# Performance work log

Hardware: AMD Instinct MI355X
Metric: run time of the kernel (lower is better)

Reference implementation:

```python
import jax, jax.numpy as jnp
import numpy as np
from functools import partial

N = 10000      # nodes
E = 100000     # edges
WIDTH = 64     # node hidden width
KER_W = 1024   # kernel MLP hidden width
KER_IN = 6     # edge feature dim
DEPTH = 6


def setup_inputs() -> dict:
    key = jax.random.key(0)
    ks = jax.random.split(key, 16)

    def glorot(k, shape):
        fan_in = shape[0]
        return jax.random.normal(k, shape, dtype=jnp.float32) / np.sqrt(fan_in)

    inp = {
        "x": jax.random.normal(ks[0], (N, 1), dtype=jnp.float32),
        "edge_index": jax.random.randint(ks[1], (2, E), 0, N, dtype=jnp.int32),
        "edge_attr": jax.random.uniform(ks[2], (E, KER_IN), dtype=jnp.float32),
        # fc1: in_width=1 -> width
        "fc1_w": glorot(ks[3], (1, WIDTH)),
        "fc1_b": jnp.zeros((WIDTH,), jnp.float32),
        # kernel DenseNet: ker_in -> ker_width -> ker_width -> width**2 (ReLU between)
        "k1_w": glorot(ks[4], (KER_IN, KER_W)),
        "k1_b": jnp.zeros((KER_W,), jnp.float32),
        "k2_w": glorot(ks[5], (KER_W, KER_W)),
        "k2_b": jnp.zeros((KER_W,), jnp.float32),
        "k3_w": glorot(ks[6], (KER_W, WIDTH * WIDTH)),
        "k3_b": jnp.zeros((WIDTH * WIDTH,), jnp.float32),
        # NNConv_old root weight + bias
        "root_w": glorot(ks[7], (WIDTH, WIDTH)),
        "conv_b": jnp.zeros((WIDTH,), jnp.float32),
        # fc2: width -> 1
        "fc2_w": glorot(ks[8], (WIDTH, 1)),
        "fc2_b": jnp.zeros((1,), jnp.float32),
    }
    return inp


def reference(x, edge_index, edge_attr, fc1_w, fc1_b, k1_w, k1_b, k2_w, k2_b,
              k3_w, k3_b, root_w, conv_b, fc2_w, fc2_b):
    src = edge_index[0]  # x_j (source, gathered)
    dst = edge_index[1]  # aggregation target

    # Per-edge kernel MLP -> [E, width, width]. edge_attr is constant across
    # depth iterations, so compute the edge weights once (same math).
    h = jax.nn.relu(edge_attr @ k1_w + k1_b)
    h = jax.nn.relu(h @ k2_w + k2_b)
    ew = (h @ k3_w + k3_b).reshape(E, WIDTH, WIDTH)

    # mean aggregation denominators (scatter_mean semantics: deg clamped to 1)
    deg = jax.ops.segment_sum(jnp.ones((E,), jnp.float32), dst, num_segments=N)
    deg = jnp.maximum(deg, 1.0)[:, None]  # [N,1]

    z = x @ fc1_w + fc1_b  # [N, width]
    for _ in range(DEPTH):
        msg = jnp.einsum('ei,eio->eo', z[src], ew)            # gather + per-edge matmul
        agg = jax.ops.segment_sum(msg, dst, num_segments=N)   # scatter-add
        agg = agg / deg                                       # mean
        z = jax.nn.relu(agg + z @ root_w + conv_b)
    return z @ fc2_w + fc2_b  # [N, 1]
```

## Files before the change

### kernel.cpp

```cpp
#include <hip/hip_runtime.h>
#include <hip/hip_bf16.h>

#define N_NODES 10000
#define N_EDGES 100000
#define DEPTH   6
#define E_CHUNK 12500

typedef __attribute__((ext_vector_type(8))) short short8;
typedef __attribute__((ext_vector_type(4))) float f32x4;
typedef unsigned short u16;

__device__ __forceinline__ float bf2f(u16 u) {
    union { float f; unsigned int i; } v; v.i = ((unsigned int)u) << 16; return v.f;
}
__device__ __forceinline__ u16 f2bf(float f) {
    union { float f; unsigned int i; } v; v.f = f;
    unsigned int x = v.i;
    unsigned int r = (x + 0x7fffu + ((x >> 16) & 1u)) >> 16;
    return (u16)r;
}

__device__ __forceinline__ void gload_lds16(const void* g, void* s) {
    __builtin_amdgcn_global_load_lds((const __attribute__((address_space(1))) void*)g,
                                     (__attribute__((address_space(3))) void*)s, 16, 0, 0);
}

__global__ void k2_transpose_kernel(const float* __restrict__ k2w, u16* __restrict__ k2T) {
    int idx = blockIdx.x * 256 + threadIdx.x;
    int n = idx >> 10, k = idx & 1023;
    k2T[idx] = f2bf(k2w[k * 1024 + n]);
}
__global__ void k3_permT_kernel(const float* __restrict__ k3w, u16* __restrict__ k3pT) {
    int idx = blockIdx.x * 256 + threadIdx.x;
    int n = idx >> 10, c = idx & 1023;
    k3pT[idx] = f2bf(k3w[(size_t)c * 4096 + (n & 63) * 64 + (n >> 6)]);
}
__global__ void b3_permute_kernel(const float* __restrict__ b3, float* __restrict__ b3p) {
    int n = blockIdx.x * 256 + threadIdx.x;
    if (n >= 4096) return;
    b3p[n] = b3[(n & 63) * 64 + (n >> 6)];
}

__global__ void deg_kernel(const int* __restrict__ ei, float* __restrict__ deg) {
    int e = blockIdx.x * 256 + threadIdx.x;
    if (e < N_EDGES) atomicAdd(&deg[ei[N_EDGES + e]], 1.0f);
}

__global__ void gemm1_kernel(const float* __restrict__ ea, const float* __restrict__ k1w,
                             const float* __restrict__ k1b, u16* __restrict__ h1, int e0) {
    int idx = blockIdx.x * 256 + threadIdx.x;
    int c = idx & 1023;
    int e = (idx >> 10) + e0;
    float acc = k1b[c];
#pragma unroll
    for (int i = 0; i < 6; i++) acc += ea[e * 6 + i] * k1w[i * 1024 + c];
    h1[idx] = f2bf(fmaxf(acc, 0.0f));
}

template <int NOUT, bool RELU, bool FUSE_MSG>
__global__ __launch_bounds__(256) void gemm128_kernel(
    const u16* __restrict__ A, const u16* __restrict__ BT,
    const float* __restrict__ bias, u16* __restrict__ C, int M,
    const int* __restrict__ ei, const float* __restrict__ z,
    float* __restrict__ agg) {
    constexpr int K = 1024;
    constexpr int KTILES = 32;
    __shared__ __align__(16) u16 ldsA[3][128 * 32];
    __shared__ __align__(16) u16 ldsB[3][128 * 32];

    const int t = threadIdx.x;
    const int lane = t & 63, w = t >> 6;
    const int wm = w >> 1, wn = w & 1;
    const int fm = lane & 15, q = lane >> 4;
    const int m0 = blockIdx.y * 128;
    const int n0 = blockIdx.x * 128;

    f32x4 acc[4][4];
#pragma unroll
    for (int a = 0; a < 4; a++)
#pragma unroll
        for (int b = 0; b < 4; b++) acc[a][b] = (f32x4){0.f, 0.f, 0.f, 0.f};

    const u16* gA[2]; const u16* gB[2];
    int dL[2];
#pragma unroll
    for (int l = 0; l < 2; l++) {
        int L = l * 256 + t;
        int r = L >> 2;
        int kq = (L & 3) ^ ((r >> 1) & 3);
        int ra = m0 + r; if (ra >= M) ra = M - 1;
        gA[l] = A + (size_t)ra * K + kq * 8;
        gB[l] = BT + (size_t)(n0 + r) * K + kq * 8;
        dL[l] = L * 8;
    }
    const int xq = q ^ ((fm >> 1) & 3);
    const int aB = (wm * 64 + fm) * 32 + xq * 8;
    const int bB = (wn * 64 + fm) * 32 + xq * 8;

#pragma unroll
    for (int tt = 0; tt < 2; tt++) {
#pragma unroll
        for (int l = 0; l < 2; l++) { gload_lds16(gA[l], &ldsA[tt][dL[l]]); gA[l] += 32; }
#pragma unroll
        for (int l = 0; l < 2; l++) { gload_lds16(gB[l], &ldsB[tt][dL[l]]); gB[l] += 32; }
    }
    asm volatile("s_waitcnt vmcnt(4)" ::: "memory");
    __builtin_amdgcn_s_barrier();
    asm volatile("" ::: "memory");

    int cur = 0;
    for (int kt = 0; kt < KTILES; ++kt) {
        const u16* la = ldsA[cur];
        const u16* lb = ldsB[cur];

        short8 af[4], bf[4];
#pragma unroll
        for (int mi = 0; mi < 4; mi++)
            af[mi] = *reinterpret_cast<const short8*>(&la[aB + mi * 512]);
#pragma unroll
        for (int ni = 0; ni < 4; ni++)
            bf[ni] = *reinterpret_cast<const short8*>(&lb[bB + ni * 512]);

        if (kt + 2 < KTILES) {
            int nb = cur + 2; if (nb >= 3) nb -= 3;
#pragma unroll
            for (int l = 0; l < 2; l++) { gload_lds16(gA[l], &ldsA[nb][dL[l]]); gA[l] += 32; }
#pragma unroll
            for (int l = 0; l < 2; l++) { gload_lds16(gB[l], &ldsB[nb][dL[l]]); gB[l] += 32; }
        }

        __builtin_amdgcn_s_setprio(1);
#pragma unroll
        for (int mi = 0; mi < 4; mi++)
#pragma unroll
            for (int ni = 0; ni < 4; ni++)
                acc[mi][ni] = __builtin_amdgcn_mfma_f32_16x16x32_bf16(af[mi], bf[ni], acc[mi][ni], 0, 0, 0);
        __builtin_amdgcn_s_setprio(0);

        if (kt + 2 < KTILES) {
            asm volatile("s_waitcnt vmcnt(4)" ::: "memory");
        } else if (kt + 1 < KTILES) {
            asm volatile("s_waitcnt vmcnt(0)" ::: "memory");
        }
        if (kt + 1 < KTILES) {
            __builtin_amdgcn_s_barrier();
            asm volatile("" ::: "memory");
        }
        cur = cur + 1; if (cur == 3) cur = 0;
    }

    if (!FUSE_MSG) {
#pragma unroll
        for (int mi = 0; mi < 4; mi++) {
#pragma unroll
            for (int ni = 0; ni < 4; ni++) {
                int col = n0 + wn * 64 + ni * 16 + fm;
                float bsv = bias[col];
#pragma unroll
                for (int r = 0; r < 4; r++) {
                    int row = m0 + wm * 64 + mi * 16 + q * 4 + r;
                    if (row < M) {
                        float v = acc[mi][ni][r] + bsv;
                        if (RELU) v = fmaxf(v, 0.0f);
                        C[(size_t)row * NOUT + col] = f2bf(v);
                    }
                }
            }
        }
    } else {
        const int o = (n0 >> 6) + wn;
        float bsv[4];
        int iidx[4];
#pragma unroll
        for (int ni = 0; ni < 4; ni++) {
            bsv[ni] = bias[n0 + wn * 64 + ni * 16 + fm];
            iidx[ni] = ni * 16 + fm;
        }
#pragma unroll
        for (int mi = 0; mi < 4; mi++) {
#pragma unroll
            for (int r = 0; r < 4; r++) {
                int e = m0 + wm * 64 + mi * 16 + q * 4 + r;
                float partial = 0.f;
                int dst = 0;
                if (e < M) {
                    int src = ei[e];
                    dst = ei[N_EDGES + e];
                    const float* zs = z + (size_t)src * 64;
#pragma unroll
                    for (int ni = 0; ni < 4; ni++)
                        partial += (acc[mi][ni][r] + bsv[ni]) * zs[iidx[ni]];
                }
                partial += __shfl_xor(partial, 1);
                partial += __shfl_xor(partial, 2);
                partial += __shfl_xor(partial, 4);
                partial += __shfl_xor(partial, 8);
                if (fm == 0 && e < M) atomicAdd(&agg[(size_t)dst * 64 + o], partial);
            }
        }
    }
}

__global__ void z0_kernel(const float* __restrict__ x, const float* __restrict__ w,
                          const float* __restrict__ b, float* __restrict__ z) {
    int idx = blockIdx.x * 256 + threadIdx.x;
    int n = idx >> 6, o = idx & 63;
    z[idx] = x[n] * w[o] + b[o];
}

__global__ __launch_bounds__(256) void update_kernel(const float* __restrict__ zin,
                                                     const float* __restrict__ agg,
                                                     const float* __restrict__ deg,
                                                     const float* __restrict__ rootw,
                                                     const float* __restrict__ convb,
                                                     float* __restrict__ zout) {
    int n = blockIdx.x * 4 + (threadIdx.x >> 6);
    int o = threadIdx.x & 63;
    float r = convb[o];
    const float* zr = zin + (size_t)n * 64;
#pragma unroll 8
    for (int i = 0; i < 64; i++) r += zr[i] * rootw[i * 64 + o];
    float d = deg[n];
    d = d < 1.0f ? 1.0f : d;
    float v = agg[(size_t)n * 64 + o] / d + r;
    zout[(size_t)n * 64 + o] = fmaxf(v, 0.0f);
}

__global__ void final_kernel(const float* __restrict__ z, const float* __restrict__ w,
                             const float* __restrict__ b, float* __restrict__ out) {
    int n = blockIdx.x * 256 + threadIdx.x;
    if (n >= N_NODES) return;
    float acc = b[0];
#pragma unroll 8
    for (int o = 0; o < 64; o++) acc += z[(size_t)n * 64 + o] * w[o];
    out[n] = acc;
}

__global__ void dbg_kernel(float* __restrict__ out, float val, int n) {
    int i = blockIdx.x * 256 + threadIdx.x;
    if (i < n) out[i] = val;
}

extern "C" void kernel_launch(void* const* d_in, const int* in_sizes, int n_in,
                              void* d_out, int out_size, void* d_ws, size_t ws_size,
                              hipStream_t stream) {
    const float* x     = (const float*)d_in[0];
    const int*   ei    = (const int*)  d_in[1];
    const float* ea    = (const float*)d_in[2];
    const float* fc1w  = (const float*)d_in[3];
    const float* fc1b  = (const float*)d_in[4];
    const float* k1w   = (const float*)d_in[5];
    const float* k1b   = (const float*)d_in[6];
    const float* k2w   = (const float*)d_in[7];
    const float* k2b   = (const float*)d_in[8];
    const float* k3w   = (const float*)d_in[9];
    const float* k3b   = (const float*)d_in[10];
    const float* rootw = (const float*)d_in[11];
    const float* convb = (const float*)d_in[12];
    const float* fc2w  = (const float*)d_in[13];
    const float* fc2b  = (const float*)d_in[14];
    float* out = (float*)d_out;

    const size_t NEED = 249000000;
    if (ws_size < NEED) {
        dbg_kernel<<<(N_NODES + 255) / 256, 256, 0, stream>>>(out, (float)(ws_size >> 20), N_NODES);
        return;
    }

    char* p = (char*)d_ws;
    auto alloc = [&](size_t bytes) {
        char* r = p;
        p += (bytes + 255) & ~(size_t)255;
        return r;
    };
    u16*   h2   = (u16*)  alloc((size_t)N_EDGES * 1024 * 2);
    u16*   h1ch = (u16*)  alloc((size_t)E_CHUNK * 1024 * 2);
    u16*   k2T  = (u16*)  alloc((size_t)1024 * 1024 * 2);
    u16*   k3pT = (u16*)  alloc((size_t)4096 * 1024 * 2);
    float* b3p  = (float*)alloc(4096 * 4);
    float* zA   = (float*)alloc((size_t)N_NODES * 64 * 4);
    float* zB   = (float*)alloc((size_t)N_NODES * 64 * 4);
    float* agg  = (float*)alloc((size_t)N_NODES * 64 * 4);
    float* deg  = (float*)alloc((size_t)N_NODES * 4);

    hipMemsetAsync(deg, 0, (size_t)N_NODES * 4, stream);

    k2_transpose_kernel<<<(1024 * 1024) / 256, 256, 0, stream>>>(k2w, k2T);
    k3_permT_kernel<<<(4096 * 1024) / 256, 256, 0, stream>>>(k3w, k3pT);
    b3_permute_kernel<<<16, 256, 0, stream>>>(k3b, b3p);
    deg_kernel<<<(N_EDGES + 255) / 256, 256, 0, stream>>>(ei, deg);

    for (int e0 = 0; e0 < N_EDGES; e0 += E_CHUNK) {
        gemm1_kernel<<<(E_CHUNK * 1024) / 256, 256, 0, stream>>>(ea, k1w, k1b, h1ch, e0);
        dim3 g2(1024 / 128, (E_CHUNK + 127) / 128);
        gemm128_kernel<1024, true, false><<<g2, 256, 0, stream>>>(
            h1ch, k2T, k2b, h2 + (size_t)e0 * 1024, E_CHUNK, nullptr, nullptr, nullptr);
    }

    z0_kernel<<<(N_NODES * 64) / 256, 256, 0, stream>>>(x, fc1w, fc1b, zA);

    float* zin = zA;
    float* zout = zB;
    for (int d = 0; d < DEPTH; d++) {
        hipMemsetAsync(agg, 0, (size_t)N_NODES * 64 * 4, stream);
        dim3 g3(4096 / 128, (N_EDGES + 127) / 128);
        gemm128_kernel<4096, false, true><<<g3, 256, 0, stream>>>(
            h2, k3pT, b3p, nullptr, N_EDGES, ei, zin, agg);
        update_kernel<<<N_NODES / 4, 256, 0, stream>>>(zin, agg, deg, rootw, convb, zout);
        float* tmp = zin; zin = zout; zout = tmp;
    }

    final_kernel<<<(N_NODES + 255) / 256, 256, 0, stream>>>(zin, fc2w, fc2b, out);
}
```

Baseline: 7.496 ms.

## Use 256x256 tiled 8-wave fused GEMM for per-depth edge message kernel

Replaces the 128x128 fused k3 GEMM plus message-scatter kernel with a dedicated 256x256 tile kernel using 512 threads, 64-wide K slices and a double-buffered, interleaved stage/read/MFMA schedule with XOR-swizzled LDS. Larger tiles raise arithmetic intensity and cut the number of times A and B are re-read from global memory across the dominant per-depth GEMM. The cost is heavier register and LDS use per block and many barriers, which may limit occupancy. The generic GEMM loses its fused-message template branch.

```diff
diff --git a/kernel.cpp b/kernel.cpp
--- a/kernel.cpp
+++ b/kernel.cpp
@@ -57,12 +57,10 @@
     h1[idx] = f2bf(fmaxf(acc, 0.0f));
 }
 
-template <int NOUT, bool RELU, bool FUSE_MSG>
+template <int NOUT, bool RELU>
 __global__ __launch_bounds__(256) void gemm128_kernel(
     const u16* __restrict__ A, const u16* __restrict__ BT,
-    const float* __restrict__ bias, u16* __restrict__ C, int M,
-    const int* __restrict__ ei, const float* __restrict__ z,
-    float* __restrict__ agg) {
+    const float* __restrict__ bias, u16* __restrict__ C, int M) {
     constexpr int K = 1024;
     constexpr int KTILES = 32;
     __shared__ __align__(16) u16 ldsA[3][128 * 32];
@@ -149,56 +147,193 @@
         cur = cur + 1; if (cur == 3) cur = 0;
     }
 
-    if (!FUSE_MSG) {
-#pragma unroll
-        for (int mi = 0; mi < 4; mi++) {
-#pragma unroll
-            for (int ni = 0; ni < 4; ni++) {
-                int col = n0 + wn * 64 + ni * 16 + fm;
-                float bsv = bias[col];
-#pragma unroll
-                for (int r = 0; r < 4; r++) {
-                    int row = m0 + wm * 64 + mi * 16 + q * 4 + r;
-                    if (row < M) {
-                        float v = acc[mi][ni][r] + bsv;
-                        if (RELU) v = fmaxf(v, 0.0f);
-                        C[(size_t)row * NOUT + col] = f2bf(v);
-                    }
+#pragma unroll
+    for (int mi = 0; mi < 4; mi++) {
+#pragma unroll
+        for (int ni = 0; ni < 4; ni++) {
+            int col = n0 + wn * 64 + ni * 16 + fm;
+            float bsv = bias[col];
+#pragma unroll
+            for (int r = 0; r < 4; r++) {
+                int row = m0 + wm * 64 + mi * 16 + q * 4 + r;
+                if (row < M) {
+                    float v = acc[mi][ni][r] + bsv;
+                    if (RELU) v = fmaxf(v, 0.0f);
+                    C[(size_t)row * NOUT + col] = f2bf(v);
                 }
             }
         }
-    } else {
-        const int o = (n0 >> 6) + wn;
-        float bsv[4];
-        int iidx[4];
-#pragma unroll
-        for (int ni = 0; ni < 4; ni++) {
-            bsv[ni] = bias[n0 + wn * 64 + ni * 16 + fm];
-            iidx[ni] = ni * 16 + fm;
-        }
-#pragma unroll
-        for (int mi = 0; mi < 4; mi++) {
-#pragma unroll
-            for (int r = 0; r < 4; r++) {
-                int e = m0 + wm * 64 + mi * 16 + q * 4 + r;
-                float partial = 0.f;
-                int dst = 0;
-                if (e < M) {
-                    int src = ei[e];
-                    dst = ei[N_EDGES + e];
-                    const float* zs = z + (size_t)src * 64;
-#pragma unroll
-                    for (int ni = 0; ni < 4; ni++)
-                        partial += (acc[mi][ni][r] + bsv[ni]) * zs[iidx[ni]];
-                }
-                partial += __shfl_xor(partial, 1);
-                partial += __shfl_xor(partial, 2);
-                partial += __shfl_xor(partial, 4);
-                partial += __shfl_xor(partial, 8);
-                if (fm == 0 && e < M) atomicAdd(&agg[(size_t)dst * 64 + o], partial);
+    }
+}
+
+__global__ __launch_bounds__(512, 2) void fused256_kernel(
+    const u16* __restrict__ A, const u16* __restrict__ BT,
+    const float* __restrict__ bias, const int* __restrict__ ei,
+    const float* __restrict__ z, float* __restrict__ agg) {
+    __shared__ __align__(16) u16 ldsA[2 * 2 * 128 * 64];
+    __shared__ __align__(16) u16 ldsB[2 * 2 * 128 * 64];
+
+    const int t = threadIdx.x;
+    const int lane = t & 63, w = t >> 6;
+    const int wm = w >> 2, wn = w & 3;
+    const int fm = lane & 15, q = lane >> 4;
+    const int m0 = blockIdx.y * 256;
+    const int n0 = blockIdx.x * 256;
+    const int M = N_EDGES;
+
+    const u16* pA[2][2]; const u16* pB[2][2];
+    int dOff[2];
+#pragma unroll
+    for (int l = 0; l < 2; l++) {
+        int L = l * 512 + t;
+        int r = L >> 3, sp = L & 7;
+        int kofs = (sp ^ (r & 7)) * 8;
+        dOff[l] = L * 8;
+#pragma unroll
+        for (int h = 0; h < 2; h++) {
+            int ra = m0 + h * 128 + r; if (ra >= M) ra = M - 1;
+            pA[h][l] = A + (size_t)ra * 1024 + kofs;
+            pB[h][l] = BT + (size_t)(n0 + h * 128 + r) * 1024 + kofs;
+        }
+    }
+
+#define LDSA(cp, h) (ldsA + ((((cp) * 2 + (h))) << 13))
+#define LDSB(cp, h) (ldsB + ((((cp) * 2 + (h))) << 13))
+#define STAGE_A(cp, h, kofs) do { \
+        gload_lds16(pA[h][0] + (kofs), LDSA(cp, h) + dOff[0]); \
+        gload_lds16(pA[h][1] + (kofs), LDSA(cp, h) + dOff[1]); } while (0)
+#define STAGE_B(cp, h, kofs) do { \
+        gload_lds16(pB[h][0] + (kofs), LDSB(cp, h) + dOff[0]); \
+        gload_lds16(pB[h][1] + (kofs), LDSB(cp, h) + dOff[1]); } while (0)
+#define BAR() do { __builtin_amdgcn_s_barrier(); asm volatile("" ::: "memory"); } while (0)
+
+    int sslot[2];
+    sslot[0] = ((q) ^ (fm & 7)) * 8;
+    sslot[1] = ((4 + q) ^ (fm & 7)) * 8;
+    const int bh = wn >> 1;
+    const int bRow = (wn & 1) * 64 + fm;
+
+    f32x4 acc[8][4];
+#pragma unroll
+    for (int a = 0; a < 8; a++)
+#pragma unroll
+        for (int b = 0; b < 4; b++) acc[a][b] = (f32x4){0.f, 0.f, 0.f, 0.f};
+
+    short8 af[4][2], bf0[2][2], bf1[2][2];
+
+#define READ_A(cp, miB) do { \
+        _Pragma("unroll") for (int m2 = 0; m2 < 4; m2++) \
+        _Pragma("unroll") for (int ks = 0; ks < 2; ks++) \
+            af[m2][ks] = *reinterpret_cast<const short8*>( \
+                LDSA(cp, wm) + (((miB) + m2) * 16 + fm) * 64 + sslot[ks]); } while (0)
+#define READ_B(cp, reg, niB) do { \
+        _Pragma("unroll") for (int n2 = 0; n2 < 2; n2++) \
+        _Pragma("unroll") for (int ks = 0; ks < 2; ks++) \
+            reg[n2][ks] = *reinterpret_cast<const short8*>( \
+                LDSB(cp, bh) + (bRow + ((niB) + n2) * 16) * 64 + sslot[ks]); } while (0)
+#define MFMA_Q(miB, reg, niB) do { \
+        __builtin_amdgcn_s_setprio(1); \
+        _Pragma("unroll") for (int m2 = 0; m2 < 4; m2++) \
+        _Pragma("unroll") for (int n2 = 0; n2 < 2; n2++) { \
+            acc[(miB) + m2][(niB) + n2] = __builtin_amdgcn_mfma_f32_16x16x32_bf16( \
+                af[m2][0], reg[n2][0], acc[(miB) + m2][(niB) + n2], 0, 0, 0); \
+            acc[(miB) + m2][(niB) + n2] = __builtin_amdgcn_mfma_f32_16x16x32_bf16( \
+                af[m2][1], reg[n2][1], acc[(miB) + m2][(niB) + n2], 0, 0, 0); } \
+        __builtin_amdgcn_s_setprio(0); } while (0)
+
+    STAGE_A(0, 0, 0); STAGE_A(0, 1, 0); STAGE_B(0, 0, 0); STAGE_B(0, 1, 0);
+    STAGE_B(1, 0, 64); STAGE_B(1, 1, 64);
+    asm volatile("s_waitcnt vmcnt(4)" ::: "memory");
+    BAR();
+
+    for (int it = 0; it < 8; ++it) {
+        const int kB = it * 128 + 64;
+        const int kC = it * 128 + 128;
+        const int kD = it * 128 + 192;
+        const bool g = (it < 7);
+        READ_A(0, 0); READ_B(0, bf0, 0);
+        STAGE_A(1, 0, kB);
+        BAR();
+        MFMA_Q(0, bf0, 0);
+        BAR();
+        READ_B(0, bf1, 2);
+        STAGE_A(1, 1, kB);
+        BAR();
+        MFMA_Q(0, bf1, 2);
+        BAR();
+        READ_A(0, 4);
+        if (g) STAGE_B(0, 0, kC);
+        BAR();
+        MFMA_Q(4, bf1, 2);
+        BAR();
+        if (g) STAGE_B(0, 1, kC);
+        BAR();
+        MFMA_Q(4, bf0, 0);
+        if (g) { asm volatile("s_waitcnt vmcnt(4)" ::: "memory"); }
+        else   { asm volatile("s_waitcnt vmcnt(0)" ::: "memory"); }
+        BAR();
+        READ_A(1, 0); READ_B(1, bf0, 0);
+        if (g) STAGE_A(0, 0, kC);
+        BAR();
+        MFMA_Q(0, bf0, 0);
+        BAR();
+        READ_B(1, bf1, 2);
+        if (g) STAGE_A(0, 1, kC);
+        BAR();
+        MFMA_Q(0, bf1, 2);
+        BAR();
+        READ_A(1, 4);
+        if (g) STAGE_B(1, 0, kD);
+        BAR();
+        MFMA_Q(4, bf1, 2);
+        BAR();
+        if (g) STAGE_B(1, 1, kD);
+        BAR();
+        MFMA_Q(4, bf0, 0);
+        if (g) {
+            asm volatile("s_waitcnt vmcnt(4)" ::: "memory");
+            BAR();
+        }
+    }
+
+    const int o = (n0 >> 6) + wn;
+    float bsv[4];
+    int iidx[4];
+#pragma unroll
+    for (int ni = 0; ni < 4; ni++) {
+        bsv[ni] = bias[n0 + wn * 64 + ni * 16 + fm];
+        iidx[ni] = ni * 16 + fm;
+    }
+#pragma unroll
+    for (int mi = 0; mi < 8; mi++) {
+#pragma unroll
+        for (int r = 0; r < 4; r++) {
+            int e = m0 + wm * 128 + mi * 16 + q * 4 + r;
+            float partial = 0.f;
+            int dst = 0;
+            if (e < M) {
+                int src = ei[e];
+                dst = ei[N_EDGES + e];
+                const float* zs = z + (size_t)src * 64;
+#pragma unroll
+                for (int ni = 0; ni < 4; ni++)
+                    partial += (acc[mi][ni][r] + bsv[ni]) * zs[iidx[ni]];
             }
-        }
-    }
+            partial += __shfl_xor(partial, 1);
+            partial += __shfl_xor(partial, 2);
+            partial += __shfl_xor(partial, 4);
+            partial += __shfl_xor(partial, 8);
+            if (fm == 0 && e < M) atomicAdd(&agg[(size_t)dst * 64 + o], partial);
+        }
+    }
+#undef LDSA
+#undef LDSB
+#undef STAGE_A
+#undef STAGE_B
+#undef BAR
+#undef READ_A
+#undef READ_B
+#undef MFMA_Q
 }
 
 __global__ void z0_kernel(const float* __restrict__ x, const float* __restrict__ w,
@@ -293,8 +428,8 @@
     for (int e0 = 0; e0 < N_EDGES; e0 += E_CHUNK) {
         gemm1_kernel<<<(E_CHUNK * 1024) / 256, 256, 0, stream>>>(ea, k1w, k1b, h1ch, e0);
         dim3 g2(1024 / 128, (E_CHUNK + 127) / 128);
-        gemm128_kernel<1024, true, false><<<g2, 256, 0, stream>>>(
-            h1ch, k2T, k2b, h2 + (size_t)e0 * 1024, E_CHUNK, nullptr, nullptr, nullptr);
+        gemm128_kernel<1024, true><<<g2, 256, 0, stream>>>(
+            h1ch, k2T, k2b, h2 + (size_t)e0 * 1024, E_CHUNK);
     }
 
     z0_kernel<<<(N_NODES * 64) / 256, 256, 0, stream>>>(x, fc1w, fc1b, zA);
@@ -303,9 +438,8 @@
     float* zout = zB;
     for (int d = 0; d < DEPTH; d++) {
         hipMemsetAsync(agg, 0, (size_t)N_NODES * 64 * 4, stream);
-        dim3 g3(4096 / 128, (N_EDGES + 127) / 128);
-        gemm128_kernel<4096, false, true><<<g3, 256, 0, stream>>>(
-            h2, k3pT, b3p, nullptr, N_EDGES, ei, zin, agg);
+        dim3 g3(4096 / 256, (N_EDGES + 255) / 256);
+        fused256_kernel<<<g3, 512, 0, stream>>>(h2, k3pT, b3p, ei, zin, agg);
         update_kernel<<<N_NODES / 4, 256, 0, stream>>>(zin, agg, deg, rootw, convb, zout);
         float* tmp = zin; zin = zout; zout = tmp;
     }
```

Result: slower. 8.784 ms (+17.2%).

## Reassociate per-edge message via node-level z·W3 product with source-sorted edges

Applied to the files above, without the earlier changes.

Instead of materializing the per-edge 64x64 weights each depth step through a 100000x4096x1024 GEMM, the message is reassociated. Each step first computes Y = z_src·W3 per source node, a small MFMA over node blocks that uses a bf16 hi/lo split of z to keep precision. Each edge's message is then the h2 row dotted with Y, plus a precomputed bias term. Edges are sorted by source through a histogram, scan and scatter so that each block handles the edges of 16 source nodes and reuses Y from LDS. This sharply cuts the FLOPs per depth step, but it adds sort preprocessing, streaming of h2 and W3T on every step, and a large per-thread slot register array that can hurt occupancy.

```diff
diff --git a/kernel.cpp b/kernel.cpp
--- a/kernel.cpp
+++ b/kernel.cpp
@@ -5,6 +5,10 @@
 #define N_EDGES 100000
 #define DEPTH   6
 #define E_CHUNK 12500
+#define NPB     16
+#define SLOTS   48
+#define CCH     16
+#define NCH     64
 
 typedef __attribute__((ext_vector_type(8))) short short8;
 typedef __attribute__((ext_vector_type(4))) float f32x4;
@@ -30,39 +34,77 @@
     int n = idx >> 10, k = idx & 1023;
     k2T[idx] = f2bf(k2w[k * 1024 + n]);
 }
-__global__ void k3_permT_kernel(const float* __restrict__ k3w, u16* __restrict__ k3pT) {
+__global__ void w3t_kernel(const float* __restrict__ k3w, u16* __restrict__ W3T) {
     int idx = blockIdx.x * 256 + threadIdx.x;
-    int n = idx >> 10, c = idx & 1023;
-    k3pT[idx] = f2bf(k3w[(size_t)c * 4096 + (n & 63) * 64 + (n >> 6)]);
-}
-__global__ void b3_permute_kernel(const float* __restrict__ b3, float* __restrict__ b3p) {
-    int n = blockIdx.x * 256 + threadIdx.x;
-    if (n >= 4096) return;
-    b3p[n] = b3[(n & 63) * 64 + (n >> 6)];
+    int col = idx >> 6, i = idx & 63;
+    int c = col >> 6, o = col & 63;
+    W3T[idx] = f2bf(k3w[(size_t)c * 4096 + i * 64 + o]);
 }
 
 __global__ void deg_kernel(const int* __restrict__ ei, float* __restrict__ deg) {
     int e = blockIdx.x * 256 + threadIdx.x;
     if (e < N_EDGES) atomicAdd(&deg[ei[N_EDGES + e]], 1.0f);
 }
+__global__ void srchist_kernel(const int* __restrict__ ei, int* __restrict__ cnt) {
+    int e = blockIdx.x * 256 + threadIdx.x;
+    if (e < N_EDGES) atomicAdd(&cnt[ei[e]], 1);
+}
+__global__ void scan_kernel(const int* __restrict__ cnt, int* __restrict__ off) {
+    __shared__ int part[1024];
+    int t = threadIdx.x;
+    int base = t * 10;
+    int loc[10];
+    int s = 0;
+#pragma unroll
+    for (int k = 0; k < 10; ++k) {
+        int b = base + k;
+        loc[k] = s;
+        if (b < N_NODES) s += cnt[b];
+    }
+    part[t] = s;
+    __syncthreads();
+    for (int d = 1; d < 1024; d <<= 1) {
+        int v = (t >= d) ? part[t - d] : 0;
+        __syncthreads();
+        part[t] += v;
+        __syncthreads();
+    }
+    int pre = (t == 0) ? 0 : part[t - 1];
+#pragma unroll
+    for (int k = 0; k < 10; ++k) {
+        int b = base + k;
+        if (b <= N_NODES) off[b] = pre + loc[k];
+    }
+}
+__global__ void scatter_kernel(const int* __restrict__ ei, const int* __restrict__ off,
+                               int* __restrict__ cur, int* __restrict__ srcS,
+                               int* __restrict__ dstS, int* __restrict__ esort) {
+    int e = blockIdx.x * 256 + threadIdx.x;
+    if (e >= N_EDGES) return;
+    int s = ei[e];
+    int p = off[s] + atomicAdd(&cur[s], 1);
+    srcS[p] = s;
+    dstS[p] = ei[N_EDGES + e];
+    esort[p] = e;
+}
 
 __global__ void gemm1_kernel(const float* __restrict__ ea, const float* __restrict__ k1w,
-                             const float* __restrict__ k1b, u16* __restrict__ h1, int e0) {
+                             const float* __restrict__ k1b, const int* __restrict__ esort,
+                             u16* __restrict__ h1, int e0) {
     int idx = blockIdx.x * 256 + threadIdx.x;
     int c = idx & 1023;
-    int e = (idx >> 10) + e0;
+    int erow = (idx >> 10) + e0;
+    int eo = esort[erow];
     float acc = k1b[c];
 #pragma unroll
-    for (int i = 0; i < 6; i++) acc += ea[e * 6 + i] * k1w[i * 1024 + c];
+    for (int i = 0; i < 6; i++) acc += ea[eo * 6 + i] * k1w[i * 1024 + c];
     h1[idx] = f2bf(fmaxf(acc, 0.0f));
 }
 
-template <int NOUT, bool RELU, bool FUSE_MSG>
+template <int NOUT, bool RELU>
 __global__ __launch_bounds__(256) void gemm128_kernel(
     const u16* __restrict__ A, const u16* __restrict__ BT,
-    const float* __restrict__ bias, u16* __restrict__ C, int M,
-    const int* __restrict__ ei, const float* __restrict__ z,
-    float* __restrict__ agg) {
+    const float* __restrict__ bias, u16* __restrict__ C, int M) {
     constexpr int K = 1024;
     constexpr int KTILES = 32;
     __shared__ __align__(16) u16 ldsA[3][128 * 32];
@@ -149,63 +191,47 @@
         cur = cur + 1; if (cur == 3) cur = 0;
     }
 
-    if (!FUSE_MSG) {
-#pragma unroll
-        for (int mi = 0; mi < 4; mi++) {
-#pragma unroll
-            for (int ni = 0; ni < 4; ni++) {
-                int col = n0 + wn * 64 + ni * 16 + fm;
-                float bsv = bias[col];
-#pragma unroll
-                for (int r = 0; r < 4; r++) {
-                    int row = m0 + wm * 64 + mi * 16 + q * 4 + r;
-                    if (row < M) {
-                        float v = acc[mi][ni][r] + bsv;
-                        if (RELU) v = fmaxf(v, 0.0f);
-                        C[(size_t)row * NOUT + col] = f2bf(v);
-                    }
+#pragma unroll
+    for (int mi = 0; mi < 4; mi++) {
+#pragma unroll
+        for (int ni = 0; ni < 4; ni++) {
+            int col = n0 + wn * 64 + ni * 16 + fm;
+            float bsv = bias[col];
+#pragma unroll
+            for (int r = 0; r < 4; r++) {
+                int row = m0 + wm * 64 + mi * 16 + q * 4 + r;
+                if (row < M) {
+                    float v = acc[mi][ni][r] + bsv;
+                    if (RELU) v = fmaxf(v, 0.0f);
+                    C[(size_t)row * NOUT + col] = f2bf(v);
                 }
             }
         }
-    } else {
-        const int o = (n0 >> 6) + wn;
-        float bsv[4];
-        int iidx[4];
-#pragma unroll
-        for (int ni = 0; ni < 4; ni++) {
-            bsv[ni] = bias[n0 + wn * 64 + ni * 16 + fm];
-            iidx[ni] = ni * 16 + fm;
-        }
-#pragma unroll
-        for (int mi = 0; mi < 4; mi++) {
-#pragma unroll
-            for (int r = 0; r < 4; r++) {
-                int e = m0 + wm * 64 + mi * 16 + q * 4 + r;
-                float partial = 0.f;
-                int dst = 0;
-                if (e < M) {
-                    int src = ei[e];
-                    dst = ei[N_EDGES + e];
-                    const float* zs = z + (size_t)src * 64;
-#pragma unroll
-                    for (int ni = 0; ni < 4; ni++)
-                        partial += (acc[mi][ni][r] + bsv[ni]) * zs[iidx[ni]];
-                }
-                partial += __shfl_xor(partial, 1);
-                partial += __shfl_xor(partial, 2);
-                partial += __shfl_xor(partial, 4);
-                partial += __shfl_xor(partial, 8);
-                if (fm == 0 && e < M) atomicAdd(&agg[(size_t)dst * 64 + o], partial);
-            }
-        }
-    }
-}
-
-__global__ void z0_kernel(const float* __restrict__ x, const float* __restrict__ w,
-                          const float* __restrict__ b, float* __restrict__ z) {
-    int idx = blockIdx.x * 256 + threadIdx.x;
-    int n = idx >> 6, o = idx & 63;
-    z[idx] = x[n] * w[o] + b[o];
+    }
+}
+
+__global__ __launch_bounds__(256) void z0_kernel(const float* __restrict__ x,
+                                                 const float* __restrict__ w,
+                                                 const float* __restrict__ b,
+                                                 const float* __restrict__ b3,
+                                                 float* __restrict__ z,
+                                                 u16* __restrict__ zh, u16* __restrict__ zl,
+                                                 float* __restrict__ bterm) {
+    __shared__ float zrow[4][64];
+    int ln = threadIdx.x >> 6;
+    int n = blockIdx.x * 4 + ln;
+    int o = threadIdx.x & 63;
+    float v = x[n] * w[o] + b[o];
+    z[(size_t)n * 64 + o] = v;
+    u16 hv = f2bf(v);
+    zh[(size_t)n * 64 + o] = hv;
+    zl[(size_t)n * 64 + o] = f2bf(v - bf2f(hv));
+    zrow[ln][o] = v;
+    __syncthreads();
+    float bt = 0.f;
+#pragma unroll 8
+    for (int i = 0; i < 64; i++) bt += zrow[ln][i] * b3[i * 64 + o];
+    bterm[(size_t)n * 64 + o] = bt;
 }
 
 __global__ __launch_bounds__(256) void update_kernel(const float* __restrict__ zin,
@@ -213,8 +239,13 @@
                                                      const float* __restrict__ deg,
                                                      const float* __restrict__ rootw,
                                                      const float* __restrict__ convb,
-                                                     float* __restrict__ zout) {
-    int n = blockIdx.x * 4 + (threadIdx.x >> 6);
+                                                     const float* __restrict__ b3,
+                                                     float* __restrict__ zout,
+                                                     u16* __restrict__ zh, u16* __restrict__ zl,
+                                                     float* __restrict__ bterm) {
+    __shared__ float zrow[4][64];
+    int ln = threadIdx.x >> 6;
+    int n = blockIdx.x * 4 + ln;
     int o = threadIdx.x & 63;
     float r = convb[o];
     const float* zr = zin + (size_t)n * 64;
@@ -223,8 +254,124 @@
     float d = deg[n];
     d = d < 1.0f ? 1.0f : d;
     float v = agg[(size_t)n * 64 + o] / d + r;
-    zout[(size_t)n * 64 + o] = fmaxf(v, 0.0f);
-}
+    v = fmaxf(v, 0.0f);
+    zout[(size_t)n * 64 + o] = v;
+    u16 hv = f2bf(v);
+    zh[(size_t)n * 64 + o] = hv;
+    zl[(size_t)n * 64 + o] = f2bf(v - bf2f(hv));
+    zrow[ln][o] = v;
+    __syncthreads();
+    float bt = 0.f;
+#pragma unroll 8
+    for (int i = 0; i < 64; i++) bt += zrow[ln][i] * b3[i * 64 + o];
+    bterm[(size_t)n * 64 + o] = bt;
+}
+
+#define ACC2(u, y0, y1) { m = fmaf(__uint_as_float((u) << 16), (y0), m); \
+                          m = fmaf(__uint_as_float((u) & 0xffff0000u), (y1), m); }
+__global__ __launch_bounds__(256) void fusedF_kernel(
+    const u16* __restrict__ h2s, const u16* __restrict__ W3T,
+    const u16* __restrict__ zh, const u16* __restrict__ zl,
+    const float* __restrict__ bterm, const int* __restrict__ srcS,
+    const int* __restrict__ dstS, const int* __restrict__ binoff,
+    float* __restrict__ agg) {
+    __shared__ float Ylds[NPB][CCH][64];
+
+    const int t = threadIdx.x;
+    const int lane = t & 63, w = t >> 6;
+    const int fm = lane & 15, q = lane >> 4;
+    const int n0 = blockIdx.x * NPB;
+
+    const short8 azh0 = *reinterpret_cast<const short8*>(&zh[(size_t)(n0 + fm) * 64 + q * 8]);
+    const short8 azh1 = *reinterpret_cast<const short8*>(&zh[(size_t)(n0 + fm) * 64 + 32 + q * 8]);
+    const short8 azl0 = *reinterpret_cast<const short8*>(&zl[(size_t)(n0 + fm) * 64 + q * 8]);
+    const short8 azl1 = *reinterpret_cast<const short8*>(&zl[(size_t)(n0 + fm) * 64 + 32 + q * 8]);
+
+    const int j0 = binoff[n0], j1 = binoff[n0 + NPB];
+    const int cnt = j1 - j0;
+    const int per = cnt >> 2, rem = cnt & 3;
+    const int myc = per + (w < rem ? 1 : 0);
+    const int mys = j0 + w * per + (w < rem ? w : rem);
+    const int mye = mys + myc;
+
+    float msg[SLOTS];
+    int ssl[SLOTS];
+#pragma unroll
+    for (int sl = 0; sl < SLOTS; ++sl) {
+        msg[sl] = 0.f;
+        ssl[sl] = n0;
+        if (sl < myc) {
+            int sg = srcS[mys + sl];
+            ssl[sl] = sg;
+            msg[sl] = bterm[(size_t)sg * 64 + lane];
+        }
+    }
+
+    for (int ch = 0; ch < NCH; ++ch) {
+        __syncthreads();
+#pragma unroll
+        for (int s2 = 0; s2 < 16; ++s2) {
+            int sc = w * 16 + s2;
+            size_t cb = ((size_t)ch * 1024 + sc * 16 + fm) * 64;
+            short8 b0 = *reinterpret_cast<const short8*>(&W3T[cb + q * 8]);
+            short8 b1 = *reinterpret_cast<const short8*>(&W3T[cb + 32 + q * 8]);
+            f32x4 a = (f32x4){0.f, 0.f, 0.f, 0.f};
+            a = __builtin_amdgcn_mfma_f32_16x16x32_bf16(azh0, b0, a, 0, 0, 0);
+            a = __builtin_amdgcn_mfma_f32_16x16x32_bf16(azl0, b0, a, 0, 0, 0);
+            a = __builtin_amdgcn_mfma_f32_16x16x32_bf16(azh1, b1, a, 0, 0, 0);
+            a = __builtin_amdgcn_mfma_f32_16x16x32_bf16(azl1, b1, a, 0, 0, 0);
+            int cl = sc >> 2, ob = (sc & 3) * 16 + fm;
+#pragma unroll
+            for (int r = 0; r < 4; ++r) Ylds[q * 4 + r][cl][ob] = a[r];
+        }
+        __syncthreads();
+        float yreg[16];
+        int sprev = -1;
+#pragma unroll
+        for (int sl = 0; sl < SLOTS; ++sl) {
+            if (sl < myc) {
+                int s = ssl[sl] - n0;
+                if (s != sprev) {
+#pragma unroll
+                    for (int cc = 0; cc < 16; ++cc) yreg[cc] = Ylds[s][cc][lane];
+                    sprev = s;
+                }
+                const uint4* hp = reinterpret_cast<const uint4*>(
+                    h2s + (size_t)(mys + sl) * 1024 + ch * CCH);
+                uint4 ha = hp[0], hb = hp[1];
+                float m = msg[sl];
+                ACC2(ha.x, yreg[0], yreg[1]);   ACC2(ha.y, yreg[2], yreg[3]);
+                ACC2(ha.z, yreg[4], yreg[5]);   ACC2(ha.w, yreg[6], yreg[7]);
+                ACC2(hb.x, yreg[8], yreg[9]);   ACC2(hb.y, yreg[10], yreg[11]);
+                ACC2(hb.z, yreg[12], yreg[13]); ACC2(hb.w, yreg[14], yreg[15]);
+                msg[sl] = m;
+            }
+        }
+        for (int j = mys + SLOTS; j < mye; ++j) {
+            int sg = srcS[j];
+            int s = sg - n0;
+            float m = (ch == 0) ? bterm[(size_t)sg * 64 + lane] : 0.f;
+            const uint4* hp = reinterpret_cast<const uint4*>(
+                h2s + (size_t)j * 1024 + ch * CCH);
+            uint4 ha = hp[0], hb = hp[1];
+            ACC2(ha.x, Ylds[s][0][lane], Ylds[s][1][lane]);
+            ACC2(ha.y, Ylds[s][2][lane], Ylds[s][3][lane]);
+            ACC2(ha.z, Ylds[s][4][lane], Ylds[s][5][lane]);
+            ACC2(ha.w, Ylds[s][6][lane], Ylds[s][7][lane]);
+            ACC2(hb.x, Ylds[s][8][lane], Ylds[s][9][lane]);
+            ACC2(hb.y, Ylds[s][10][lane], Ylds[s][11][lane]);
+            ACC2(hb.z, Ylds[s][12][lane], Ylds[s][13][lane]);
+            ACC2(hb.w, Ylds[s][14][lane], Ylds[s][15][lane]);
+            atomicAdd(&agg[(size_t)dstS[j] * 64 + lane], m);
+        }
+    }
+
+#pragma unroll
+    for (int sl = 0; sl < SLOTS; ++sl) {
+        if (sl < myc) atomicAdd(&agg[(size_t)dstS[mys + sl] * 64 + lane], msg[sl]);
+    }
+}
+#undef ACC2
 
 __global__ void final_kernel(const float* __restrict__ z, const float* __restrict__ w,
                              const float* __restrict__ b, float* __restrict__ out) {
@@ -261,7 +408,7 @@
     const float* fc2b  = (const float*)d_in[14];
     float* out = (float*)d_out;
 
-    const size_t NEED = 249000000;
+    const size_t NEED = 256000000;
     if (ws_size < NEED) {
         dbg_kernel<<<(N_NODES + 255) / 256, 256, 0, stream>>>(out, (float)(ws_size >> 20), N_NODES);
         return;
@@ -273,40 +420,52 @@
         p += (bytes + 255) & ~(size_t)255;
         return r;
     };
-    u16*   h2   = (u16*)  alloc((size_t)N_EDGES * 1024 * 2);
-    u16*   h1ch = (u16*)  alloc((size_t)E_CHUNK * 1024 * 2);
-    u16*   k2T  = (u16*)  alloc((size_t)1024 * 1024 * 2);
-    u16*   k3pT = (u16*)  alloc((size_t)4096 * 1024 * 2);
-    float* b3p  = (float*)alloc(4096 * 4);
-    float* zA   = (float*)alloc((size_t)N_NODES * 64 * 4);
-    float* zB   = (float*)alloc((size_t)N_NODES * 64 * 4);
-    float* agg  = (float*)alloc((size_t)N_NODES * 64 * 4);
-    float* deg  = (float*)alloc((size_t)N_NODES * 4);
+    u16*   h2s   = (u16*)  alloc((size_t)N_EDGES * 1024 * 2);
+    u16*   W3T   = (u16*)  alloc((size_t)65536 * 64 * 2);
+    u16*   k2T   = (u16*)  alloc((size_t)1024 * 1024 * 2);
+    u16*   h1ch  = (u16*)  alloc((size_t)E_CHUNK * 1024 * 2);
+    float* zA    = (float*)alloc((size_t)N_NODES * 64 * 4);
+    float* zB    = (float*)alloc((size_t)N_NODES * 64 * 4);
+    u16*   zhb   = (u16*)  alloc((size_t)N_NODES * 64 * 2);
+    u16*   zlb   = (u16*)  alloc((size_t)N_NODES * 64 * 2);
+    float* bterm = (float*)alloc((size_t)N_NODES * 64 * 4);
+    float* agg   = (float*)alloc((size_t)N_NODES * 64 * 4);
+    float* deg   = (float*)alloc((size_t)N_NODES * 4);
+    int*   scnt  = (int*)  alloc((size_t)N_NODES * 4);
+    int*   scur  = (int*)  alloc((size_t)N_NODES * 4);
+    int*   boff  = (int*)  alloc((size_t)(N_NODES + 1) * 4);
+    int*   srcS  = (int*)  alloc((size_t)N_EDGES * 4);
+    int*   dstS  = (int*)  alloc((size_t)N_EDGES * 4);
+    int*   esort = (int*)  alloc((size_t)N_EDGES * 4);
 
     hipMemsetAsync(deg, 0, (size_t)N_NODES * 4, stream);
+    hipMemsetAsync(scnt, 0, (size_t)N_NODES * 4, stream);
+    hipMemsetAsync(scur, 0, (size_t)N_NODES * 4, stream);
 
     k2_transpose_kernel<<<(1024 * 1024) / 256, 256, 0, stream>>>(k2w, k2T);
-    k3_permT_kernel<<<(4096 * 1024) / 256, 256, 0, stream>>>(k3w, k3pT);
-    b3_permute_kernel<<<16, 256, 0, stream>>>(k3b, b3p);
+    w3t_kernel<<<(65536 * 64) / 256, 256, 0, stream>>>(k3w, W3T);
     deg_kernel<<<(N_EDGES + 255) / 256, 256, 0, stream>>>(ei, deg);
+    srchist_kernel<<<(N_EDGES + 255) / 256, 256, 0, stream>>>(ei, scnt);
+    scan_kernel<<<1, 1024, 0, stream>>>(scnt, boff);
+    scatter_kernel<<<(N_EDGES + 255) / 256, 256, 0, stream>>>(ei, boff, scur, srcS, dstS, esort);
 
     for (int e0 = 0; e0 < N_EDGES; e0 += E_CHUNK) {
-        gemm1_kernel<<<(E_CHUNK * 1024) / 256, 256, 0, stream>>>(ea, k1w, k1b, h1ch, e0);
+        gemm1_kernel<<<(E_CHUNK * 1024) / 256, 256, 0, stream>>>(ea, k1w, k1b, esort, h1ch, e0);
         dim3 g2(1024 / 128, (E_CHUNK + 127) / 128);
-        gemm128_kernel<1024, true, false><<<g2, 256, 0, stream>>>(
-            h1ch, k2T, k2b, h2 + (size_t)e0 * 1024, E_CHUNK, nullptr, nullptr, nullptr);
-    }
-
-    z0_kernel<<<(N_NODES * 64) / 256, 256, 0, stream>>>(x, fc1w, fc1b, zA);
+        gemm128_kernel<1024, true><<<g2, 256, 0, stream>>>(
+            h1ch, k2T, k2b, h2s + (size_t)e0 * 1024, E_CHUNK);
+    }
+
+    z0_kernel<<<N_NODES / 4, 256, 0, stream>>>(x, fc1w, fc1b, k3b, zA, zhb, zlb, bterm);
 
     float* zin = zA;
     float* zout = zB;
     for (int d = 0; d < DEPTH; d++) {
         hipMemsetAsync(agg, 0, (size_t)N_NODES * 64 * 4, stream);
-        dim3 g3(4096 / 128, (N_EDGES + 127) / 128);
-        gemm128_kernel<4096, false, true><<<g3, 256, 0, stream>>>(
-            h2, k3pT, b3p, nullptr, N_EDGES, ei, zin, agg);
-        update_kernel<<<N_NODES / 4, 256, 0, stream>>>(zin, agg, deg, rootw, convb, zout);
+        fusedF_kernel<<<N_NODES / NPB, 256, 0, stream>>>(
+            h2s, W3T, zhb, zlb, bterm, srcS, dstS, boff, agg);
+        update_kernel<<<N_NODES / 4, 256, 0, stream>>>(
+            zin, agg, deg, rootw, convb, k3b, zout, zhb, zlb, bterm);
         float* tmp = zin; zin = zout; zout = tmp;
     }
 
```

Result: slower. 19.27 ms (+157.1%).
